# Kernel tuning notes

Hardware: AMD Instinct MI355X
Metric: run time of the kernel (lower is better)

The kernel has to match this reference:

```python
import jax, jax.numpy as jnp
import numpy as np

L = 4096          # total packed length
HID = 2560        # hidden_size
H = 8             # num_attention_heads
KV = 4            # num_key_value_heads
HD = 256          # head_dim
SW = 1024         # sliding_window
SCALING = 256.0 ** -0.5  # query_pre_attn_scalar ** -0.5
EPS = 1e-6
ROPE_BASE = 10000.0


def setup_inputs() -> dict:
    key = jax.random.key(0)
    ks = jax.random.split(key, 9)
    hidden_states = jax.random.normal(ks[0], (L, HID), jnp.float32)
    Wq = jax.random.normal(ks[1], (HID, H * HD), jnp.float32) * 0.02
    Wk = jax.random.normal(ks[2], (HID, KV * HD), jnp.float32) * 0.02
    Wv = jax.random.normal(ks[3], (HID, KV * HD), jnp.float32) * 0.02
    Wo = jax.random.normal(ks[4], (H * HD, HID), jnp.float32) * 0.02
    q_norm_w = jax.random.normal(ks[5], (HD,), jnp.float32) * 0.1
    k_norm_w = jax.random.normal(ks[6], (HD,), jnp.float32) * 0.1
    # 4 packed sequences of length 1024 each; positions restart per sequence
    cu_seqlens = jnp.array([0, 1024, 2048, 3072, 4096], jnp.int32)
    pos = jnp.tile(jnp.arange(1024, dtype=jnp.float32), 4)  # [L]
    inv_freq = 1.0 / (ROPE_BASE ** (jnp.arange(0, HD, 2, dtype=jnp.float32) / HD))
    freqs = pos[:, None] * inv_freq[None, :]                # [L, HD/2]
    emb = jnp.concatenate([freqs, freqs], axis=-1)          # [L, HD]
    cos, sin = jnp.cos(emb), jnp.sin(emb)
    return {"hidden_states": hidden_states, "cos": cos, "sin": sin,
            "Wq": Wq, "Wk": Wk, "Wv": Wv, "Wo": Wo,
            "q_norm_w": q_norm_w, "k_norm_w": k_norm_w,
            "cu_seqlens": cu_seqlens}


def _rotate_half(x):
    x1, x2 = x[..., : HD // 2], x[..., HD // 2:]
    return jnp.concatenate([-x2, x1], axis=-1)


def _rms_norm(x, w):
    # Gemma3RMSNorm: x * rsqrt(mean(x^2) + eps) * (1 + w)
    x32 = x.astype(jnp.float32)
    out = x32 * jax.lax.rsqrt(jnp.mean(x32 * x32, axis=-1, keepdims=True) + EPS)
    return (out * (1.0 + w.astype(jnp.float32))).astype(x.dtype)


def _packed_sliding_causal_mask(cu_seqlens, total_len):
    pos = jnp.arange(total_len)
    seq_ids = jnp.searchsorted(cu_seqlens[1:], pos, side='right')
    seq_mask = seq_ids[:, None] == seq_ids[None, :]
    dist = pos[None, :] - pos[:, None]                      # pos[j] - pos[i]
    causal = dist <= 0
    window = dist >= -(SW - 1)                              # left_window = SW - 1
    keep = seq_mask & causal & window
    return jnp.where(keep, 0.0, -jnp.inf).astype(jnp.float32)  # [L, L]


def reference(hidden_states, cos, sin, Wq, Wk, Wv, Wo, q_norm_w, k_norm_w, cu_seqlens):
    total_len = hidden_states.shape[0]
    # projections -> [n_heads, L, head_dim]
    q = (hidden_states @ Wq).reshape(total_len, H, HD).transpose(1, 0, 2)
    k = (hidden_states @ Wk).reshape(total_len, KV, HD).transpose(1, 0, 2)
    v = (hidden_states @ Wv).reshape(total_len, KV, HD).transpose(1, 0, 2)
    q = _rms_norm(q, q_norm_w)
    k = _rms_norm(k, k_norm_w)
    # RoPE (cos/sin broadcast over heads)
    q = q * cos + _rotate_half(q) * sin
    k = k * cos + _rotate_half(k) * sin
    # GQA repeat_kv: [KV, L, HD] -> [H, L, HD]
    n_rep = H // KV
    k = jnp.repeat(k, n_rep, axis=0)
    v = jnp.repeat(v, n_rep, axis=0)
    mask = _packed_sliding_causal_mask(cu_seqlens, total_len)
    scores = jnp.einsum('hqd,hkd->hqk', q, k) * SCALING + mask[None]
    attn = jax.nn.softmax(scores.astype(jnp.float32), axis=-1).astype(q.dtype)
    out = jnp.einsum('hqk,hkd->qhd', attn, v).reshape(total_len, H * HD)
    return out @ Wo  # [L, hidden]
```

## Files before the change

### kernel.cpp

```cpp
#include <hip/hip_runtime.h>
#include <hip/hip_bf16.h>

typedef unsigned short u16;
typedef float f32x4 __attribute__((ext_vector_type(4)));
typedef short bf16x8 __attribute__((ext_vector_type(8)));

__device__ __forceinline__ float bf2f(u16 u) {
    union { float f; unsigned int i; } c; c.i = ((unsigned int)u) << 16; return c.f;
}
__device__ __forceinline__ u16 f2bf(float f) {
    union { float f; unsigned int i; } c; c.f = f;
    unsigned int r = c.i + 0x7fffu + ((c.i >> 16) & 1u);
    return (u16)(r >> 16);
}
__device__ __forceinline__ void gload16(const void* g, void* l) {
    __builtin_amdgcn_global_load_lds(
        (const __attribute__((address_space(1))) void*)g,
        (__attribute__((address_space(3))) void*)l, 16, 0, 0);
}

__global__ __launch_bounds__(256) void convert_f32_bf16(
    const float* __restrict__ in, u16* __restrict__ out, int n8)
{
    int i = blockIdx.x * 256 + threadIdx.x;
    if (i >= n8) return;
    const float4 a = *(const float4*)&in[i * 8];
    const float4 b = *(const float4*)&in[i * 8 + 4];
    bf16x8 o;
    o[0] = (short)f2bf(a.x); o[1] = (short)f2bf(a.y);
    o[2] = (short)f2bf(a.z); o[3] = (short)f2bf(a.w);
    o[4] = (short)f2bf(b.x); o[5] = (short)f2bf(b.y);
    o[6] = (short)f2bf(b.z); o[7] = (short)f2bf(b.w);
    *(bf16x8*)&out[i * 8] = o;
}

__global__ __launch_bounds__(256) void transpose_f32_bf16(
    const float* __restrict__ in, u16* __restrict__ out, int R, int C)
{
    __shared__ u16 tile[32][34];
    const int tx = threadIdx.x & 31;
    const int ty = threadIdx.x >> 5;
    const size_t r0 = (size_t)blockIdx.y * 32;
    const size_t c0 = (size_t)blockIdx.x * 32;
#pragma unroll
    for (int i = 0; i < 4; ++i) {
        int r = ty + 8 * i;
        tile[r][tx] = f2bf(in[(r0 + r) * C + c0 + tx]);
    }
    __syncthreads();
#pragma unroll
    for (int i = 0; i < 4; ++i) {
        int r = ty + 8 * i;
        out[(c0 + r) * R + r0 + tx] = tile[tx][r];
    }
}

__global__ __launch_bounds__(256) void transpose_bf16(
    const u16* __restrict__ in, u16* __restrict__ out, int ldin, int ldout)
{
    __shared__ u16 tile[32][34];
    const int tx = threadIdx.x & 31;
    const int ty = threadIdx.x >> 5;
    const size_t r0 = (size_t)blockIdx.y * 32;
    const size_t c0 = (size_t)blockIdx.x * 32;
#pragma unroll
    for (int i = 0; i < 4; ++i) {
        int r = ty + 8 * i;
        tile[r][tx] = in[(r0 + r) * (size_t)ldin + c0 + tx];
    }
    __syncthreads();
#pragma unroll
    for (int i = 0; i < 4; ++i) {
        int r = ty + 8 * i;
        out[(c0 + r) * (size_t)ldout + r0 + tx] = tile[tx][r];
    }
}

template<typename TOUT>
__global__ __launch_bounds__(512, 2) void gemm_bt8p(
    const u16* __restrict__ A, const u16* __restrict__ Bt, TOUT* __restrict__ C,
    int M, int N, int K)
{
    __shared__ u16 As[2][2][128 * 64];
    __shared__ u16 Bs[2][2][128 * 64];
    const int tid  = threadIdx.x;
    const int lane = tid & 63;
    const int w    = tid >> 6;
    const int wm   = w >> 2;
    const int wn   = w & 3;
    const int g    = lane >> 4, c = lane & 15;

    const int nbx = gridDim.x;
    int lin = blockIdx.y * nbx + blockIdx.x;
    const int cpx = (nbx * gridDim.y) >> 3;
    lin = (lin & 7) * cpx + (lin >> 3);
    const size_t mbase = (size_t)(lin / nbx) * 256;
    const size_t nbase = (size_t)(lin % nbx) * 256;

    const int schunk = w * 2;
    const int srow0  = lane >> 3;
    const int sslot  = lane & 7;

    auto stageA = [&](int t, int half) {
        u16* dst = &As[t & 1][half][0];
        const u16* src = A + (mbase + half * 128) * (size_t)K + t * 64;
#pragma unroll
        for (int i = 0; i < 2; ++i) {
            const int ch = schunk + i;
            const int rw = ch * 8 + srow0;
            gload16(src + (size_t)rw * K + ((sslot ^ (rw & 7)) << 3), dst + ch * 512);
        }
    };
    auto stageB = [&](int t, int half) {
        u16* dst = &Bs[t & 1][half][0];
        const u16* src = Bt + (nbase + half * 128) * (size_t)K + t * 64;
#pragma unroll
        for (int i = 0; i < 2; ++i) {
            const int ch = schunk + i;
            const int rw = ch * 8 + srow0;
            gload16(src + (size_t)rw * K + ((sslot ^ (rw & 7)) << 3), dst + ch * 512);
        }
    };
    auto ldA = [&](int t, int m, int kk) -> bf16x8 {
        const int r = m * 16 + c;
        return *(const bf16x8*)&As[t & 1][wm][r * 64 + ((kk * 32 + g * 8) ^ ((r & 7) << 3))];
    };
    auto ldB = [&](int t, int n, int kk) -> bf16x8 {
        const int r = (wn & 1) * 64 + n * 16 + c;
        return *(const bf16x8*)&Bs[t & 1][wn >> 1][r * 64 + ((kk * 32 + g * 8) ^ ((r & 7) << 3))];
    };

    f32x4 acc[8][4];
#pragma unroll
    for (int m = 0; m < 8; ++m)
#pragma unroll
        for (int n = 0; n < 4; ++n) { acc[m][n][0]=0.f; acc[m][n][1]=0.f; acc[m][n][2]=0.f; acc[m][n][3]=0.f; }

    const int nT = K >> 6;

    stageA(0, 0); stageA(0, 1); stageB(0, 0); stageB(0, 1);
    asm volatile("s_waitcnt vmcnt(0)" ::: "memory");
    __builtin_amdgcn_sched_barrier(0);
    __builtin_amdgcn_s_barrier();

    for (int t = 0; t < nT; ++t) {
        bf16x8 bF[4][2], aF[2][2];
        const bool more = (t + 1 < nT);

#pragma unroll
        for (int n = 0; n < 4; ++n) { bF[n][0] = ldB(t, n, 0); bF[n][1] = ldB(t, n, 1); }
#pragma unroll
        for (int i = 0; i < 2; ++i) { aF[i][0] = ldA(t, i, 0); aF[i][1] = ldA(t, i, 1); }
        if (more) { stageA(t + 1, 0); stageA(t + 1, 1); }
        __builtin_amdgcn_s_barrier();
        __builtin_amdgcn_s_setprio(1);
#pragma unroll
        for (int kk = 0; kk < 2; ++kk)
#pragma unroll
            for (int i = 0; i < 2; ++i)
#pragma unroll
                for (int n = 0; n < 4; ++n)
                    acc[i][n] = __builtin_amdgcn_mfma_f32_16x16x32_bf16(
                        aF[i][kk], bF[n][kk], acc[i][n], 0, 0, 0);
        __builtin_amdgcn_s_setprio(0);
        __builtin_amdgcn_s_barrier();

#pragma unroll
        for (int q = 1; q < 4; ++q) {
#pragma unroll
            for (int i = 0; i < 2; ++i) { aF[i][0] = ldA(t, 2*q + i, 0); aF[i][1] = ldA(t, 2*q + i, 1); }
            if (q == 1 && more) { stageB(t + 1, 0); stageB(t + 1, 1); }
            __builtin_amdgcn_s_barrier();
            __builtin_amdgcn_s_setprio(1);
#pragma unroll
            for (int kk = 0; kk < 2; ++kk)
#pragma unroll
                for (int i = 0; i < 2; ++i)
#pragma unroll
                    for (int n = 0; n < 4; ++n)
                        acc[2*q + i][n] = __builtin_amdgcn_mfma_f32_16x16x32_bf16(
                            aF[i][kk], bF[n][kk], acc[2*q + i][n], 0, 0, 0);
            __builtin_amdgcn_s_setprio(0);
            __builtin_amdgcn_s_barrier();
        }

        asm volatile("s_waitcnt vmcnt(0)" ::: "memory");
        __builtin_amdgcn_sched_barrier(0);
        __builtin_amdgcn_s_barrier();
    }

#pragma unroll
    for (int m = 0; m < 8; ++m)
#pragma unroll
        for (int n = 0; n < 4; ++n)
#pragma unroll
            for (int i = 0; i < 4; ++i) {
                size_t r   = mbase + wm * 128 + m * 16 + g * 4 + i;
                size_t col = nbase + wn * 64 + n * 16 + c;
                if constexpr (sizeof(TOUT) == 4) C[r * (size_t)N + col] = acc[m][n][i];
                else                             C[r * (size_t)N + col] = f2bf(acc[m][n][i]);
            }
}

__global__ __launch_bounds__(256) void rmsnorm_rope(
    u16* __restrict__ buf, int ld, const float* __restrict__ wgt,
    const float* __restrict__ cosb, const float* __restrict__ sinb,
    int heads, float outscale)
{
    const int lane = threadIdx.x & 63;
    const int wv   = threadIdx.x >> 6;
    const int rid  = blockIdx.x * 4 + wv;
    const int t    = rid / heads;
    const int h    = rid - t * heads;
    u16* p = buf + (size_t)t * ld + h * 256 + lane * 4;

    ushort4 xu = *(const ushort4*)p;
    float x0 = bf2f(xu.x), x1 = bf2f(xu.y), x2 = bf2f(xu.z), x3 = bf2f(xu.w);
    float ss = x0*x0 + x1*x1 + x2*x2 + x3*x3;
#pragma unroll
    for (int msk = 1; msk < 64; msk <<= 1) ss += __shfl_xor(ss, msk);
    const float rstd = rsqrtf(ss * (1.0f / 256.0f) + 1e-6f);

    const int d0 = lane * 4;
    const float4 wv4 = *(const float4*)&wgt[d0];
    float xn0 = x0 * rstd * (1.0f + wv4.x);
    float xn1 = x1 * rstd * (1.0f + wv4.y);
    float xn2 = x2 * rstd * (1.0f + wv4.z);
    float xn3 = x3 * rstd * (1.0f + wv4.w);

    float pn0 = __shfl_xor(xn0, 32);
    float pn1 = __shfl_xor(xn1, 32);
    float pn2 = __shfl_xor(xn2, 32);
    float pn3 = __shfl_xor(xn3, 32);
    const float sgn = (lane < 32) ? -1.0f : 1.0f;

    const float4 cv = *(const float4*)&cosb[(size_t)t * 256 + d0];
    const float4 sv = *(const float4*)&sinb[(size_t)t * 256 + d0];
    float r0 = (xn0 * cv.x + sgn * pn0 * sv.x) * outscale;
    float r1 = (xn1 * cv.y + sgn * pn1 * sv.y) * outscale;
    float r2 = (xn2 * cv.z + sgn * pn2 * sv.z) * outscale;
    float r3 = (xn3 * cv.w + sgn * pn3 * sv.w) * outscale;

    ushort4 ou;
    ou.x = f2bf(r0); ou.y = f2bf(r1); ou.z = f2bf(r2); ou.w = f2bf(r3);
    *(ushort4*)p = ou;
}

__global__ __launch_bounds__(512, 2) void attn_kernel(
    const u16* __restrict__ q, int ldq,
    const u16* __restrict__ k, int ldk,
    const u16* __restrict__ vT,
    u16* __restrict__ Opart,
    float* __restrict__ stats)
{
    __shared__ u16 Ks[2][32 * 256];
    __shared__ u16 Vs[256 * 40];
    __shared__ u16 P[8][16][56];
    __shared__ float corrsF[8][16];
    const int tid  = threadIdx.x;
    const int lane = tid & 63;
    const int w    = tid >> 6;
    const int g    = lane >> 4, c = lane & 15;
    const int qt   = 15 - blockIdx.x;
    const int s    = blockIdx.y;
    const int kvh  = blockIdx.z & 3;
    const int kvs  = blockIdx.z >> 2;
    const int h    = kvh * 2 + (w >> 2);
    const int seq0 = s << 10;
    const int qrow0 = qt * 64 + (w & 3) * 16;
    const float NEG = -3.0e38f;

    bf16x8 qf[8];
    {
        const u16* qp = q + (size_t)(seq0 + qrow0 + c) * ldq + h * 256 + g * 8;
#pragma unroll
        for (int ch = 0; ch < 8; ++ch) qf[ch] = *(const bf16x8*)(qp + ch * 32);
    }

    const int kchunk0  = w * 2;
    const int krow_in  = (lane >> 5);
    const int kcol_lin = (lane & 31) * 16;
    const u16* kbase = k + (size_t)seq0 * ldk + kvh * 256;
    const int vd  = tid & 255;
    const int vj0 = (tid >> 8) * 2;
    const int vsw = (vd >> 3) & 3;
    const u16* vbase = vT + ((size_t)kvh * 256 + vd) * 4096 + seq0 + vj0 * 8;

    f32x4 oacc[16];
#pragma unroll
    for (int dt = 0; dt < 16; ++dt) { oacc[dt][0]=0.f; oacc[dt][1]=0.f; oacc[dt][2]=0.f; oacc[dt][3]=0.f; }
    float mq = -1e30f;
    float lq = 0.f;

    const int nt = qt + 1;
    const int t0 = kvs * nt;

    bf16x8 vreg[2];
#pragma unroll
    for (int i = 0; i < 2; ++i) {
        const int chunk = kchunk0 + i;
        const int row   = chunk * 2 + krow_in;
        const int bcol  = kcol_lin ^ ((row & 7) << 4);
        gload16(kbase + (size_t)(t0 * 32 + row) * ldk + (bcol >> 1), &Ks[0][chunk * 512]);
    }
#pragma unroll
    for (int j = 0; j < 2; ++j) vreg[j] = *(const bf16x8*)(vbase + t0 * 32 + j * 8);
    __syncthreads();
#pragma unroll
    for (int j = 0; j < 2; ++j)
        *(bf16x8*)&Vs[vd * 40 + (((vj0 + j) ^ vsw) * 8)] = vreg[j];
    __syncthreads();

    for (int ti = 0; ti < nt; ++ti) {
        const int p   = ti & 1;
        const int kv0 = (t0 + ti) * 32;

        if (ti + 1 < nt) {
#pragma unroll
            for (int i = 0; i < 2; ++i) {
                const int chunk = kchunk0 + i;
                const int row   = chunk * 2 + krow_in;
                const int bcol  = kcol_lin ^ ((row & 7) << 4);
                gload16(kbase + (size_t)(kv0 + 32 + row) * ldk + (bcol >> 1),
                        &Ks[p ^ 1][chunk * 512]);
            }
#pragma unroll
            for (int j = 0; j < 2; ++j) vreg[j] = *(const bf16x8*)(vbase + kv0 + 32 + j * 8);
        }

        f32x4 sacc[2];
#pragma unroll
        for (int nh = 0; nh < 2; ++nh) { sacc[nh][0]=0.f; sacc[nh][1]=0.f; sacc[nh][2]=0.f; sacc[nh][3]=0.f; }
        __builtin_amdgcn_s_setprio(1);
#pragma unroll
        for (int nh = 0; nh < 2; ++nh) {
            const int krow = nh * 16 + c;
#pragma unroll
            for (int ch = 0; ch < 8; ++ch) {
                const int sw = ((ch * 64 + g * 16) ^ ((c & 7) << 4)) >> 1;
                bf16x8 kf = *(const bf16x8*)&Ks[p][krow * 256 + sw];
                sacc[nh] = __builtin_amdgcn_mfma_f32_16x16x32_bf16(kf, qf[ch], sacc[nh], 0, 0, 0);
            }
        }
        __builtin_amdgcn_s_setprio(0);

        const int qloc = qrow0 + c;
        float pmax = NEG;
#pragma unroll
        for (int nh = 0; nh < 2; ++nh)
#pragma unroll
            for (int i = 0; i < 4; ++i) {
                if (kv0 + nh * 16 + g * 4 + i > qloc) sacc[nh][i] = NEG;
                pmax = fmaxf(pmax, sacc[nh][i]);
            }
        pmax = fmaxf(pmax, __shfl_xor(pmax, 16));
        pmax = fmaxf(pmax, __shfl_xor(pmax, 32));

        const bool rescale = !__all(pmax - mq <= 8.0f);
        float corr = 1.0f;
        if (rescale) {
            const float mn = fmaxf(mq, pmax);
            corr = __expf(mq - mn);
            mq = mn;
            if (g == 0) corrsF[w][c] = corr;
        }

        float rowsum = 0.f;
        unsigned int pw[4];
#pragma unroll
        for (int nh = 0; nh < 2; ++nh) {
            float p0 = __expf(sacc[nh][0] - mq);
            float p1 = __expf(sacc[nh][1] - mq);
            float p2 = __expf(sacc[nh][2] - mq);
            float p3 = __expf(sacc[nh][3] - mq);
            rowsum += (p0 + p1) + (p2 + p3);
            pw[nh * 2 + 0] = (unsigned int)f2bf(p0) | ((unsigned int)f2bf(p1) << 16);
            pw[nh * 2 + 1] = (unsigned int)f2bf(p2) | ((unsigned int)f2bf(p3) << 16);
        }
#pragma unroll
        for (int nh = 0; nh < 2; ++nh) {
            *(unsigned int*)&P[w][c][nh * 16 + g * 4]     = pw[nh * 2 + 0];
            *(unsigned int*)&P[w][c][nh * 16 + g * 4 + 2] = pw[nh * 2 + 1];
        }
        rowsum += __shfl_xor(rowsum, 16);
        rowsum += __shfl_xor(rowsum, 32);
        lq = lq * corr + rowsum;

        bf16x8 pf = *(const bf16x8*)&P[w][c][g * 8];

        if (rescale) {
            const f32x4 c4 = *(const f32x4*)&corrsF[w][g * 4];
#pragma unroll
            for (int dt = 0; dt < 16; ++dt)
#pragma unroll
                for (int i = 0; i < 4; ++i) oacc[dt][i] *= c4[i];
        }

        __builtin_amdgcn_s_setprio(1);
#pragma unroll
        for (int dt = 0; dt < 16; ++dt) {
            const int d = dt * 16 + c;
            bf16x8 vf = *(const bf16x8*)&Vs[d * 40 + ((g ^ ((d >> 3) & 3)) * 8)];
            oacc[dt] = __builtin_amdgcn_mfma_f32_16x16x32_bf16(pf, vf, oacc[dt], 0, 0, 0);
        }
        __builtin_amdgcn_s_setprio(0);

        __syncthreads();
        if (ti + 1 < nt) {
#pragma unroll
            for (int j = 0; j < 2; ++j)
                *(bf16x8*)&Vs[vd * 40 + (((vj0 + j) ^ vsw) * 8)] = vreg[j];
        }
        __syncthreads();
    }

    u16* op = Opart + (size_t)kvs * 4096 * 2048;
#pragma unroll
    for (int dt = 0; dt < 16; ++dt)
#pragma unroll
        for (int i = 0; i < 4; ++i)
            op[(size_t)(seq0 + qrow0 + g * 4 + i) * 2048 + h * 256 + dt * 16 + c] =
                f2bf(oacc[dt][i]);
    if (g == 0) {
        const int row = seq0 + qrow0 + c;
        stats[(((size_t)kvs * 8 + h) * 2 + 0) * 4096 + row] = mq;
        stats[(((size_t)kvs * 8 + h) * 2 + 1) * 4096 + row] = lq;
    }
}

__global__ __launch_bounds__(256) void merge_partial(
    const u16* __restrict__ Op,
    const float* __restrict__ stats,
    u16* __restrict__ ob)
{
    const int idx = blockIdx.x * 256 + threadIdx.x;
    const int row = idx >> 8;
    const int col = (idx & 255) * 8;
    const int h   = col >> 8;
    const float m0 = stats[((0 * 8 + h) * 2 + 0) * 4096 + row];
    const float l0 = stats[((0 * 8 + h) * 2 + 1) * 4096 + row];
    const float m1 = stats[((1 * 8 + h) * 2 + 0) * 4096 + row];
    const float l1 = stats[((1 * 8 + h) * 2 + 1) * 4096 + row];
    const float mm = fmaxf(m0, m1);
    const float w0 = __expf(m0 - mm);
    const float w1 = __expf(m1 - mm);
    const float inv = 1.0f / (w0 * l0 + w1 * l1);
    const float s0 = w0 * inv, s1 = w1 * inv;
    const size_t base = (size_t)row * 2048 + col;
    bf16x8 a = *(const bf16x8*)&Op[base];
    bf16x8 b = *(const bf16x8*)&Op[(size_t)4096 * 2048 + base];
    bf16x8 r;
#pragma unroll
    for (int j = 0; j < 8; ++j)
        r[j] = (short)f2bf(bf2f((u16)a[j]) * s0 + bf2f((u16)b[j]) * s1);
    *(bf16x8*)&ob[base] = r;
}

extern "C" void kernel_launch(void* const* d_in, const int* in_sizes, int n_in,
                              void* d_out, int out_size, void* d_ws, size_t ws_size,
                              hipStream_t stream)
{
    const float* hid  = (const float*)d_in[0];
    const float* cosb = (const float*)d_in[1];
    const float* sinb = (const float*)d_in[2];
    const float* Wq   = (const float*)d_in[3];
    const float* Wk   = (const float*)d_in[4];
    const float* Wv   = (const float*)d_in[5];
    const float* Wo   = (const float*)d_in[6];
    const float* qnw  = (const float*)d_in[7];
    const float* knw  = (const float*)d_in[8];

    char* ws = (char*)d_ws;
    const size_t R1 = 0;
    const size_t R2 = (size_t)4096 * 2560 * 2;
    const size_t R3 = R2 * 2;
    u16* hidb  = (u16*)(ws + R1);
    u16* WoT   = (u16*)(ws + R1);
    u16* vT    = (u16*)(ws + R1 + (size_t)2560 * 2048 * 2);
    u16* WqkvT = (u16*)(ws + R2);
    u16* ob    = (u16*)(ws + R2);
    u16* qkv   = (u16*)(ws + R3);
    float* stats = (float*)(ws + R3 + (size_t)4096 * 4096 * 2);
    u16* Opart = (u16*)d_out;
    (void)ws_size; (void)in_sizes; (void)n_in; (void)out_size;

    dim3 B(256);
    convert_f32_bf16<<<dim3(4096 * 2560 / 8 / 256), B, 0, stream>>>(hid, hidb, 4096 * 2560 / 8);
    transpose_f32_bf16<<<dim3(2048 / 32, 2560 / 32), B, 0, stream>>>(Wq, WqkvT, 2560, 2048);
    transpose_f32_bf16<<<dim3(1024 / 32, 2560 / 32), B, 0, stream>>>(Wk, WqkvT + (size_t)2048 * 2560, 2560, 1024);
    transpose_f32_bf16<<<dim3(1024 / 32, 2560 / 32), B, 0, stream>>>(Wv, WqkvT + (size_t)3072 * 2560, 2560, 1024);

    gemm_bt8p<u16><<<dim3(16, 16), dim3(512), 0, stream>>>(hidb, WqkvT, qkv, 4096, 4096, 2560);

    transpose_f32_bf16<<<dim3(2560 / 32, 2048 / 32), B, 0, stream>>>(Wo, WoT, 2048, 2560);

    rmsnorm_rope<<<dim3(8192), B, 0, stream>>>(qkv, 4096, qnw, cosb, sinb, 8, 0.0625f);
    rmsnorm_rope<<<dim3(4096), B, 0, stream>>>(qkv + 2048, 4096, knw, cosb, sinb, 4, 1.0f);

    transpose_bf16<<<dim3(1024 / 32, 4096 / 32), B, 0, stream>>>(qkv + 3072, vT, 4096, 4096);

    attn_kernel<<<dim3(16, 4, 8), dim3(512), 0, stream>>>(qkv, 4096, qkv + 2048, 4096, vT,
                                                          Opart, stats);
    merge_partial<<<dim3(4096), B, 0, stream>>>(Opart, stats, ob);

    gemm_bt8p<float><<<dim3(10, 16), dim3(512), 0, stream>>>(ob, WoT, (float*)d_out, 4096, 2560, 2048);
}
```

Before: 297.5 us.

## Switch GEMM to 256x128 tiles with triple-buffered LDS prefetch

Replaces the 256x256 double-buffered GEMM with a 256x128 tile kernel that keeps three LDS stages and prefetches two K-steps ahead, waiting with partial vmcnt counts instead of draining all loads every iteration. The grids double, which gives more blocks for the 256 CUs and halves the accumulators held per thread. The cost is lower reuse of A per block, so more global traffic. Attention blocks are also reordered so the second KV split walks query tiles in ascending order, spreading the causal work more evenly.

```diff
diff --git a/kernel.cpp b/kernel.cpp
--- a/kernel.cpp
+++ b/kernel.cpp
@@ -77,17 +77,17 @@
 }
 
 template<typename TOUT>
-__global__ __launch_bounds__(512, 2) void gemm_bt8p(
+__global__ __launch_bounds__(512, 2) void gemm_bt3r(
     const u16* __restrict__ A, const u16* __restrict__ Bt, TOUT* __restrict__ C,
     int M, int N, int K)
 {
-    __shared__ u16 As[2][2][128 * 64];
-    __shared__ u16 Bs[2][2][128 * 64];
+    __shared__ u16 As[3][256 * 64];
+    __shared__ u16 Bs[3][128 * 64];
     const int tid  = threadIdx.x;
     const int lane = tid & 63;
     const int w    = tid >> 6;
-    const int wm   = w >> 2;
-    const int wn   = w & 3;
+    const int wm   = w >> 1;
+    const int wn   = w & 1;
     const int g    = lane >> 4, c = lane & 15;
 
     const int nbx = gridDim.x;
@@ -95,63 +95,66 @@
     const int cpx = (nbx * gridDim.y) >> 3;
     lin = (lin & 7) * cpx + (lin >> 3);
     const size_t mbase = (size_t)(lin / nbx) * 256;
-    const size_t nbase = (size_t)(lin % nbx) * 256;
-
-    const int schunk = w * 2;
-    const int srow0  = lane >> 3;
-    const int sslot  = lane & 7;
-
-    auto stageA = [&](int t, int half) {
-        u16* dst = &As[t & 1][half][0];
-        const u16* src = A + (mbase + half * 128) * (size_t)K + t * 64;
-#pragma unroll
-        for (int i = 0; i < 2; ++i) {
-            const int ch = schunk + i;
+    const size_t nbase = (size_t)(lin % nbx) * 128;
+
+    const int srow0 = lane >> 3;
+    const int sslot = lane & 7;
+
+    auto stageA = [&](int t, int reg) {
+        u16* dst = &As[reg][0];
+        const u16* src = A + mbase * (size_t)K + t * 64;
+#pragma unroll
+        for (int i = 0; i < 4; ++i) {
+            const int ch = w * 4 + i;
             const int rw = ch * 8 + srow0;
             gload16(src + (size_t)rw * K + ((sslot ^ (rw & 7)) << 3), dst + ch * 512);
         }
     };
-    auto stageB = [&](int t, int half) {
-        u16* dst = &Bs[t & 1][half][0];
-        const u16* src = Bt + (nbase + half * 128) * (size_t)K + t * 64;
+    auto stageB = [&](int t, int reg) {
+        u16* dst = &Bs[reg][0];
+        const u16* src = Bt + nbase * (size_t)K + t * 64;
 #pragma unroll
         for (int i = 0; i < 2; ++i) {
-            const int ch = schunk + i;
+            const int ch = w * 2 + i;
             const int rw = ch * 8 + srow0;
             gload16(src + (size_t)rw * K + ((sslot ^ (rw & 7)) << 3), dst + ch * 512);
         }
     };
-    auto ldA = [&](int t, int m, int kk) -> bf16x8 {
-        const int r = m * 16 + c;
-        return *(const bf16x8*)&As[t & 1][wm][r * 64 + ((kk * 32 + g * 8) ^ ((r & 7) << 3))];
+    auto ldA = [&](int reg, int m, int kk) -> bf16x8 {
+        const int r = wm * 64 + m * 16 + c;
+        return *(const bf16x8*)&As[reg][r * 64 + ((kk * 32 + g * 8) ^ ((r & 7) << 3))];
     };
-    auto ldB = [&](int t, int n, int kk) -> bf16x8 {
-        const int r = (wn & 1) * 64 + n * 16 + c;
-        return *(const bf16x8*)&Bs[t & 1][wn >> 1][r * 64 + ((kk * 32 + g * 8) ^ ((r & 7) << 3))];
+    auto ldB = [&](int reg, int n, int kk) -> bf16x8 {
+        const int r = wn * 64 + n * 16 + c;
+        return *(const bf16x8*)&Bs[reg][r * 64 + ((kk * 32 + g * 8) ^ ((r & 7) << 3))];
     };
 
-    f32x4 acc[8][4];
-#pragma unroll
-    for (int m = 0; m < 8; ++m)
+    f32x4 acc[4][4];
+#pragma unroll
+    for (int m = 0; m < 4; ++m)
 #pragma unroll
         for (int n = 0; n < 4; ++n) { acc[m][n][0]=0.f; acc[m][n][1]=0.f; acc[m][n][2]=0.f; acc[m][n][3]=0.f; }
 
     const int nT = K >> 6;
 
-    stageA(0, 0); stageA(0, 1); stageB(0, 0); stageB(0, 1);
-    asm volatile("s_waitcnt vmcnt(0)" ::: "memory");
+    stageA(0, 0); stageB(0, 0);
+    stageA(1, 1); stageB(1, 1);
+    asm volatile("s_waitcnt vmcnt(6)" ::: "memory");
     __builtin_amdgcn_sched_barrier(0);
     __builtin_amdgcn_s_barrier();
-
+    __builtin_amdgcn_sched_barrier(0);
+
+    int rt = 0;
     for (int t = 0; t < nT; ++t) {
+        const int rn = (rt >= 1) ? rt - 1 : rt + 2;
         bf16x8 bF[4][2], aF[2][2];
-        const bool more = (t + 1 < nT);
-
-#pragma unroll
-        for (int n = 0; n < 4; ++n) { bF[n][0] = ldB(t, n, 0); bF[n][1] = ldB(t, n, 1); }
-#pragma unroll
-        for (int i = 0; i < 2; ++i) { aF[i][0] = ldA(t, i, 0); aF[i][1] = ldA(t, i, 1); }
-        if (more) { stageA(t + 1, 0); stageA(t + 1, 1); }
+        const bool more = (t + 2 < nT);
+
+#pragma unroll
+        for (int n = 0; n < 4; ++n) { bF[n][0] = ldB(rt, n, 0); bF[n][1] = ldB(rt, n, 1); }
+#pragma unroll
+        for (int i = 0; i < 2; ++i) { aF[i][0] = ldA(rt, i, 0); aF[i][1] = ldA(rt, i, 1); }
+        if (more) stageA(t + 2, rn);
         __builtin_amdgcn_s_barrier();
         __builtin_amdgcn_s_setprio(1);
 #pragma unroll
@@ -166,36 +169,38 @@
         __builtin_amdgcn_s_barrier();
 
 #pragma unroll
-        for (int q = 1; q < 4; ++q) {
-#pragma unroll
-            for (int i = 0; i < 2; ++i) { aF[i][0] = ldA(t, 2*q + i, 0); aF[i][1] = ldA(t, 2*q + i, 1); }
-            if (q == 1 && more) { stageB(t + 1, 0); stageB(t + 1, 1); }
+        for (int i = 0; i < 2; ++i) { aF[i][0] = ldA(rt, 2 + i, 0); aF[i][1] = ldA(rt, 2 + i, 1); }
+        if (more) stageB(t + 2, rn);
+        __builtin_amdgcn_s_barrier();
+        __builtin_amdgcn_s_setprio(1);
+#pragma unroll
+        for (int kk = 0; kk < 2; ++kk)
+#pragma unroll
+            for (int i = 0; i < 2; ++i)
+#pragma unroll
+                for (int n = 0; n < 4; ++n)
+                    acc[2 + i][n] = __builtin_amdgcn_mfma_f32_16x16x32_bf16(
+                        aF[i][kk], bF[n][kk], acc[2 + i][n], 0, 0, 0);
+        __builtin_amdgcn_s_setprio(0);
+        __builtin_amdgcn_s_barrier();
+
+        if (t + 1 < nT) {
+            if (more) asm volatile("s_waitcnt vmcnt(6)" ::: "memory");
+            else      asm volatile("s_waitcnt vmcnt(0)" ::: "memory");
+            __builtin_amdgcn_sched_barrier(0);
             __builtin_amdgcn_s_barrier();
-            __builtin_amdgcn_s_setprio(1);
-#pragma unroll
-            for (int kk = 0; kk < 2; ++kk)
-#pragma unroll
-                for (int i = 0; i < 2; ++i)
-#pragma unroll
-                    for (int n = 0; n < 4; ++n)
-                        acc[2*q + i][n] = __builtin_amdgcn_mfma_f32_16x16x32_bf16(
-                            aF[i][kk], bF[n][kk], acc[2*q + i][n], 0, 0, 0);
-            __builtin_amdgcn_s_setprio(0);
-            __builtin_amdgcn_s_barrier();
-        }
-
-        asm volatile("s_waitcnt vmcnt(0)" ::: "memory");
-        __builtin_amdgcn_sched_barrier(0);
-        __builtin_amdgcn_s_barrier();
-    }
-
-#pragma unroll
-    for (int m = 0; m < 8; ++m)
+            __builtin_amdgcn_sched_barrier(0);
+        }
+        rt = (rt == 2) ? 0 : rt + 1;
+    }
+
+#pragma unroll
+    for (int m = 0; m < 4; ++m)
 #pragma unroll
         for (int n = 0; n < 4; ++n)
 #pragma unroll
             for (int i = 0; i < 4; ++i) {
-                size_t r   = mbase + wm * 128 + m * 16 + g * 4 + i;
+                size_t r   = mbase + wm * 64 + m * 16 + g * 4 + i;
                 size_t col = nbase + wn * 64 + n * 16 + c;
                 if constexpr (sizeof(TOUT) == 4) C[r * (size_t)N + col] = acc[m][n][i];
                 else                             C[r * (size_t)N + col] = f2bf(acc[m][n][i]);
@@ -261,10 +266,10 @@
     const int lane = tid & 63;
     const int w    = tid >> 6;
     const int g    = lane >> 4, c = lane & 15;
-    const int qt   = 15 - blockIdx.x;
     const int s    = blockIdx.y;
     const int kvh  = blockIdx.z & 3;
     const int kvs  = blockIdx.z >> 2;
+    const int qt   = kvs ? (int)blockIdx.x : 15 - (int)blockIdx.x;
     const int h    = kvh * 2 + (w >> 2);
     const int seq0 = s << 10;
     const int qrow0 = qt * 64 + (w & 3) * 16;
@@ -490,7 +495,7 @@
     transpose_f32_bf16<<<dim3(1024 / 32, 2560 / 32), B, 0, stream>>>(Wk, WqkvT + (size_t)2048 * 2560, 2560, 1024);
     transpose_f32_bf16<<<dim3(1024 / 32, 2560 / 32), B, 0, stream>>>(Wv, WqkvT + (size_t)3072 * 2560, 2560, 1024);
 
-    gemm_bt8p<u16><<<dim3(16, 16), dim3(512), 0, stream>>>(hidb, WqkvT, qkv, 4096, 4096, 2560);
+    gemm_bt3r<u16><<<dim3(32, 16), dim3(512), 0, stream>>>(hidb, WqkvT, qkv, 4096, 4096, 2560);
 
     transpose_f32_bf16<<<dim3(2560 / 32, 2048 / 32), B, 0, stream>>>(Wo, WoT, 2048, 2560);
 
@@ -503,5 +508,5 @@
                                                           Opart, stats);
     merge_partial<<<dim3(4096), B, 0, stream>>>(Opart, stats, ob);
 
-    gemm_bt8p<float><<<dim3(10, 16), dim3(512), 0, stream>>>(ob, WoT, (float*)d_out, 4096, 2560, 2048);
-}
+    gemm_bt3r<float><<<dim3(20, 16), dim3(512), 0, stream>>>(ob, WoT, (float*)d_out, 4096, 2560, 2048);
+}
```

Measured after the change: 304.3 us. 1.02x slower.
